# Optimization experiments

Hardware: AMD Instinct MI355X
Metric: run time of the kernel (lower is better)

The kernel has to match this reference:

```python
import jax, jax.numpy as jnp
import numpy as np

NUM_CLUSTERS = 5000  # labels.max()+1, fixed statically for jit
B, K, D, N = 256, 64, 2048, 50000
NHID, H2, NCLASS = 512, 256, 2


def setup_inputs() -> dict:
    key = jax.random.key(0)
    ks = jax.random.split(key, 16)
    s = lambda f_in: 1.0 / np.sqrt(f_in)
    return {
        "indexes": jax.random.randint(ks[0], (B,), 0, N),
        "features": jax.random.normal(ks[1], (N, D), dtype=jnp.float32),
        "labels": jax.random.randint(ks[2], (N,), 0, NUM_CLUSTERS),
        "domain": 1,
        "ori_0": 0,
        "ori_knn_neighbor": jax.random.randint(ks[3], (B, K), 0, N),
        "all_pred": jax.random.normal(ks[4], (B, K, NCLASS), dtype=jnp.float32),
        # GraphConv params (L-GCN style: weight [2*in, out])
        "W1": jax.random.normal(ks[5], (2 * D, NHID), jnp.float32) * s(2 * D),
        "b1": jnp.zeros((NHID,), jnp.float32),
        "W2": jax.random.normal(ks[6], (2 * NHID, H2), jnp.float32) * s(2 * NHID),
        "b2": jnp.zeros((H2,), jnp.float32),
        # classifier: Linear(256,256) -> PReLU(256) -> Linear(256,2)
        "Wc1": jax.random.normal(ks[7], (H2, H2), jnp.float32) * s(H2),
        "bc1": jnp.zeros((H2,), jnp.float32),
        "prelu_a": jnp.full((H2,), 0.25, jnp.float32),
        "Wc2": jax.random.normal(ks[8], (H2, NCLASS), jnp.float32) * s(H2),
        "bc2": jnp.zeros((NCLASS,), jnp.float32),
    }


def _gconv(x, A, W, b):
    # MeanAggregator: bmm(A, x); GraphConv: relu(cat([x, Ax]) @ W + b)
    agg = jnp.einsum('bkj,bjd->bkd', A, x)
    cat = jnp.concatenate([x, agg], axis=-1)
    return jax.nn.relu(jnp.einsum('bkd,df->bkf', cat, W) + b)


def reference(indexes, features, labels, domain, ori_0, ori_knn_neighbor, all_pred,
              W1, b1, W2, b2, Wc1, bc1, prelu_a, Wc2, bc2):
    # ---- cluster mean features (torch: index_add_ then divide; no_grad) ----
    clu_sum = jax.ops.segment_sum(features, labels, num_segments=NUM_CLUSTERS)
    nums = jax.ops.segment_sum(jnp.ones((features.shape[0],), features.dtype),
                               labels, num_segments=NUM_CLUSTERS)
    clu_mean = clu_sum / jnp.maximum(nums, 1.0)[:, None]  # [C, D]

    # ---- batched per-query subgraph construction (vectorized over B) ----
    clu_lab = labels[ori_knn_neighbor]            # [B, K]
    clu_feat = clu_mean[clu_lab]                  # [B, K, D]
    clu_feat = clu_feat.at[:, 0, :].set(features[indexes])  # pivot = raw feature

    A = jnp.einsum('bkd,bjd->bkj', clu_feat, clu_feat)       # pairwise similarity
    A = A * jnp.exp(all_pred[:, :, 1])[:, None, :]           # confidence weighting
    A = jax.nn.softmax(A, axis=-1)                           # row-normalized adjacency

    x = clu_feat / jnp.linalg.norm(clu_feat, axis=-1, keepdims=True)
    x = x - x[:, 0:1, :]                                     # center on pivot

    # (entire construction above is under torch.no_grad)
    x = jax.lax.stop_gradient(x)
    A = jax.lax.stop_gradient(A)

    # ---- GCN layers + classifier ----
    x = _gconv(x, A, W1, b1)      # [B, K, 512]
    x = _gconv(x, A, W2, b2)      # [B, K, 256]
    x0 = x.reshape(-1, H2)        # [B*K, 256]
    h = x0 @ Wc1 + bc1
    h = jnp.where(h >= 0, h, prelu_a * h)  # PReLU(256)
    logits = h @ Wc2 + bc2                 # [B*K, 2]

    # output_feat=True branch
    simm = jnp.sum(clu_mean * clu_mean, axis=1)                   # [C]
    pred = jax.nn.softmax(logits.reshape(B, K, NCLASS), axis=2)   # [B, K, 2]
    return (pred, simm)
```

## Files before the change

kernel.cpp:

```cpp
#include <hip/hip_runtime.h>
#include <math.h>

#define Bq 256
#define Kn 64
#define Dd 2048
#define Nn 50000
#define Cc 5000
#define NHID 512
#define H2d 256
#define LDH 264
#define MP 5376
#define PIVROW 5120
#define LDA1 72

typedef __attribute__((ext_vector_type(8))) __bf16 bf16x8;
typedef __attribute__((ext_vector_type(4))) float f32x4;

__device__ __forceinline__ unsigned short f2bf(float f) {
    union { float f; unsigned int u; } v;
    v.f = f;
    unsigned int u = v.u;
    unsigned int r = (u + 0x7fff + ((u >> 16) & 1)) >> 16;
    return (unsigned short)r;
}
__device__ __forceinline__ float bf2f(unsigned short h) {
    union { unsigned int u; float f; } v;
    v.u = ((unsigned int)h) << 16;
    return v.f;
}

__global__ void k_zero_multi(int* __restrict__ p0, int n0,
                             int* __restrict__ p1, int n1,
                             int* __restrict__ p2, int n2,
                             int* __restrict__ p3, int n3) {
    int i = blockIdx.x * 256 + threadIdx.x;
    if (i < n0) { p0[i] = 0; return; }
    i -= n0;
    if (i < n1) { p1[i] = 0; return; }
    i -= n1;
    if (i < n2) { p2[i] = 0; return; }
    i -= n2;
    if (i < n3) p3[i] = 0;
}

__global__ void k_count(const int* __restrict__ labels, int* __restrict__ cnt, int n) {
    int i = blockIdx.x * 256 + threadIdx.x;
    if (i < n) atomicAdd(&cnt[labels[i]], 1);
}

__global__ void k_alloc(const int* __restrict__ cnt, int* __restrict__ off,
                        int* __restrict__ pos, int* __restrict__ total, int C) {
    int c = blockIdx.x * 256 + threadIdx.x;
    if (c < C) {
        int o = atomicAdd(total, cnt[c]);
        off[c] = o;
        pos[c] = o;
    }
}

__global__ void k_scatter(const int* __restrict__ labels, int* __restrict__ pos,
                          int* __restrict__ rowidx, int n) {
    int i = blockIdx.x * 256 + threadIdx.x;
    if (i < n) {
        int p = atomicAdd(&pos[labels[i]], 1);
        rowidx[p] = i;
    }
}

__global__ __launch_bounds__(256) void k_meansimm(
    const float* __restrict__ feat, const int* __restrict__ rowidx,
    const int* __restrict__ off, const int* __restrict__ cnt,
    const int* __restrict__ indexes,
    float* __restrict__ clu_mean, float* __restrict__ simm,
    unsigned short* __restrict__ PA) {
    int c = blockIdx.x;
    int t = threadIdx.x;
    __shared__ float red[256];

    if (c >= Cc) {
        int b = c - Cc;
        const float* row = feat + (size_t)indexes[b] * Dd;
        float4 v0 = *(const float4*)(row + t * 4);
        float4 v1 = *(const float4*)(row + 1024 + t * 4);
        float ss = v0.x * v0.x + v0.y * v0.y + v0.z * v0.z + v0.w * v0.w +
                   v1.x * v1.x + v1.y * v1.y + v1.z * v1.z + v1.w * v1.w;
        red[t] = ss;
        __syncthreads();
        for (int s2 = 128; s2 > 0; s2 >>= 1) {
            if (t < s2) red[t] += red[t + s2];
            __syncthreads();
        }
        float tot = red[0];
        float rnn = (tot > 0.f) ? rsqrtf(tot) : 0.f;
        ushort4 c0, c1;
        c0.x = f2bf(v0.x * rnn); c0.y = f2bf(v0.y * rnn);
        c0.z = f2bf(v0.z * rnn); c0.w = f2bf(v0.w * rnn);
        c1.x = f2bf(v1.x * rnn); c1.y = f2bf(v1.y * rnn);
        c1.z = f2bf(v1.z * rnn); c1.w = f2bf(v1.w * rnn);
        unsigned short* cr = PA + (size_t)(PIVROW + b) * Dd;
        *(ushort4*)(cr + t * 4) = c0;
        *(ushort4*)(cr + 1024 + t * 4) = c1;
        return;
    }

    int n = cnt[c], st = off[c];
    float4 a0 = {0.f, 0.f, 0.f, 0.f}, a1 = {0.f, 0.f, 0.f, 0.f};
    for (int r = 0; r < n; r++) {
        const float* row = feat + (size_t)rowidx[st + r] * Dd;
        float4 v0 = *(const float4*)(row + t * 4);
        float4 v1 = *(const float4*)(row + 1024 + t * 4);
        a0.x += v0.x; a0.y += v0.y; a0.z += v0.z; a0.w += v0.w;
        a1.x += v1.x; a1.y += v1.y; a1.z += v1.z; a1.w += v1.w;
    }
    float sc = 1.f / (float)(n > 1 ? n : 1);
    a0.x *= sc; a0.y *= sc; a0.z *= sc; a0.w *= sc;
    a1.x *= sc; a1.y *= sc; a1.z *= sc; a1.w *= sc;
    float* outr = clu_mean + (size_t)c * Dd;
    *(float4*)(outr + t * 4) = a0;
    *(float4*)(outr + 1024 + t * 4) = a1;
    float ss = a0.x * a0.x + a0.y * a0.y + a0.z * a0.z + a0.w * a0.w +
               a1.x * a1.x + a1.y * a1.y + a1.z * a1.z + a1.w * a1.w;
    red[t] = ss;
    __syncthreads();
    for (int s2 = 128; s2 > 0; s2 >>= 1) {
        if (t < s2) red[t] += red[t + s2];
        __syncthreads();
    }
    if (t == 0) simm[c] = red[0];
    float tot = red[0];
    float rnn = (tot > 0.f) ? rsqrtf(tot) : 0.f;
    ushort4 c0, c1;
    c0.x = f2bf(a0.x * rnn); c0.y = f2bf(a0.y * rnn);
    c0.z = f2bf(a0.z * rnn); c0.w = f2bf(a0.w * rnn);
    c1.x = f2bf(a1.x * rnn); c1.y = f2bf(a1.y * rnn);
    c1.z = f2bf(a1.z * rnn); c1.w = f2bf(a1.w * rnn);
    unsigned short* cr = PA + (size_t)c * Dd;
    *(ushort4*)(cr + t * 4) = c0;
    *(ushort4*)(cr + 1024 + t * 4) = c1;
}

__global__ __launch_bounds__(512) void k_build_ax(
    const float* __restrict__ feat, const float* __restrict__ clu_mean,
    const int* __restrict__ labels, const int* __restrict__ indexes,
    const int* __restrict__ knn, const float* __restrict__ all_pred,
    float* __restrict__ Abuf) {
    __shared__ unsigned short Hs[64 * LDH];
    __shared__ unsigned short Ls[64 * LDH];
    __shared__ float Gs[64 * 65];
    __shared__ const float* rowp[64];
    __shared__ float wj64[64];

    int b = blockIdx.x, tid = threadIdx.x;
    int wave = tid >> 6, lane = tid & 63, quad = lane >> 4, l16 = lane & 15;
    int rs = (wave >> 1) * 16;
    int cpair = (wave & 1) * 2;

    if (tid < 64) {
        const float* p = (tid == 0) ? feat + (size_t)indexes[b] * Dd
                                    : clu_mean + (size_t)labels[knn[b * 64 + tid]] * Dd;
        rowp[tid] = p;
        wj64[tid] = expf(all_pred[(b * 64 + tid) * 2 + 1]);
    }
    __syncthreads();

    f32x4 acc[2];
#pragma unroll
    for (int j = 0; j < 2; j++) acc[j] = (f32x4){0.f, 0.f, 0.f, 0.f};

    for (int ch = 0; ch < 8; ch++) {
        int d0 = ch * 256;
        __syncthreads();
#pragma unroll
        for (int q = 0; q < 8; q++) {
            int e4 = tid + q * 512;
            int row = e4 >> 6;
            int c4 = (e4 & 63) * 4;
            float4 v = *(const float4*)(rowp[row] + d0 + c4);
            ushort4 h, l;
            h.x = f2bf(v.x); l.x = f2bf(v.x - bf2f(h.x));
            h.y = f2bf(v.y); l.y = f2bf(v.y - bf2f(h.y));
            h.z = f2bf(v.z); l.z = f2bf(v.z - bf2f(h.z));
            h.w = f2bf(v.w); l.w = f2bf(v.w - bf2f(h.w));
            *(ushort4*)&Hs[row * LDH + c4] = h;
            *(ushort4*)&Ls[row * LDH + c4] = l;
        }
        __syncthreads();
#pragma unroll
        for (int ks = 0; ks < 8; ks++) {
            int kk = ks * 32 + quad * 8;
            bf16x8 ah = *(const bf16x8*)&Hs[(rs + l16) * LDH + kk];
            bf16x8 al = *(const bf16x8*)&Ls[(rs + l16) * LDH + kk];
#pragma unroll
            for (int j = 0; j < 2; j++) {
                int jg = cpair + j;
                bf16x8 bh = *(const bf16x8*)&Hs[(jg * 16 + l16) * LDH + kk];
                bf16x8 bl = *(const bf16x8*)&Ls[(jg * 16 + l16) * LDH + kk];
                acc[j] = __builtin_amdgcn_mfma_f32_16x16x32_bf16(ah, bh, acc[j], 0, 0, 0);
                acc[j] = __builtin_amdgcn_mfma_f32_16x16x32_bf16(ah, bl, acc[j], 0, 0, 0);
                acc[j] = __builtin_amdgcn_mfma_f32_16x16x32_bf16(al, bh, acc[j], 0, 0, 0);
            }
        }
    }
    __syncthreads();
#pragma unroll
    for (int j = 0; j < 2; j++)
#pragma unroll
        for (int r = 0; r < 4; r++)
            Gs[(rs + quad * 4 + r) * 65 + (cpair + j) * 16 + l16] = acc[j][r];
    __syncthreads();
    {
        int r = tid >> 3, s = tid & 7;
        float e[8];
        float mx = -1e30f;
#pragma unroll
        for (int c8 = 0; c8 < 8; c8++) {
            int c = s * 8 + c8;
            float v = Gs[r * 65 + c] * wj64[c];
            e[c8] = v;
            mx = fmaxf(mx, v);
        }
        mx = fmaxf(mx, __shfl_xor(mx, 1, 64));
        mx = fmaxf(mx, __shfl_xor(mx, 2, 64));
        mx = fmaxf(mx, __shfl_xor(mx, 4, 64));
        float sum = 0.f;
#pragma unroll
        for (int c8 = 0; c8 < 8; c8++) {
            e[c8] = expf(e[c8] - mx);
            sum += e[c8];
        }
        sum += __shfl_xor(sum, 1, 64);
        sum += __shfl_xor(sum, 2, 64);
        sum += __shfl_xor(sum, 4, 64);
        float inv = 1.f / sum;
        float* Arow = Abuf + ((size_t)b * 64 + r) * 64;
#pragma unroll
        for (int c8 = 0; c8 < 8; c8++) Arow[s * 8 + c8] = e[c8] * inv;
    }
}

__device__ __forceinline__ void pack_item(const float* __restrict__ W,
                                          unsigned short* __restrict__ Bp,
                                          int K, int Nhalf, int split, int idx) {
    int Ntot = split ? 2 * Nhalf : Nhalf;
    int kb = idx / Ntot;
    int n = idx - kb * Ntot;
    float v[8];
#pragma unroll
    for (int j = 0; j < 8; j++) {
        int k = kb * 8 + j;
        if (split)
            v[j] = (n < Nhalf) ? W[(size_t)k * Nhalf + n]
                               : W[(size_t)(K + k) * Nhalf + (n - Nhalf)];
        else
            v[j] = W[(size_t)k * Nhalf + n];
    }
    ushort4 lo, hi;
    lo.x = f2bf(v[0]); lo.y = f2bf(v[1]); lo.z = f2bf(v[2]); lo.w = f2bf(v[3]);
    hi.x = f2bf(v[4]); hi.y = f2bf(v[5]); hi.z = f2bf(v[6]); hi.w = f2bf(v[7]);
    *(ushort4*)&Bp[(size_t)idx * 8] = lo;
    *(ushort4*)&Bp[(size_t)idx * 8 + 4] = hi;
}

__global__ __launch_bounds__(256) void k_pack_all(
    const float* __restrict__ W1, const float* __restrict__ W2,
    const float* __restrict__ Wc1, unsigned short* __restrict__ Bp1,
    unsigned short* __restrict__ Bp2, unsigned short* __restrict__ Bpc) {
    int blk = blockIdx.x;
    int tid = threadIdx.x;
    if (blk < 1024) {
        pack_item(W1, Bp1, Dd, NHID, 1, blk * 256 + tid);
    } else if (blk < 1024 + 128) {
        pack_item(W2, Bp2, 2 * NHID, H2d, 0, (blk - 1024) * 256 + tid);
    } else {
        pack_item(Wc1, Bpc, H2d, H2d, 0, (blk - 1152) * 256 + tid);
    }
}

template <int EPI>
__global__ __launch_bounds__(256) void gemm_bf16_mfma(
    const unsigned short* __restrict__ A, const unsigned short* __restrict__ Bp,
    void* __restrict__ Cout, int M, int K, int N,
    const float* __restrict__ bias, const float* __restrict__ pre_a,
    const float* __restrict__ wc2, float* __restrict__ lbuf) {
    __shared__ unsigned short Asm[128 * 32];
    __shared__ unsigned short Bsm[4 * 128 * 8];
    int tid = threadIdx.x;
    int wave = tid >> 6, lane = tid & 63;
    int quad = lane >> 4, l16 = lane & 15;
    int m0 = blockIdx.y * 128, n0 = blockIdx.x * 128;
    int wm = (wave >> 1) * 64, wn = (wave & 1) * 64;

    f32x4 acc[4][4];
#pragma unroll
    for (int i = 0; i < 4; i++)
#pragma unroll
        for (int j = 0; j < 4; j++) acc[i][j] = (f32x4){0.f, 0.f, 0.f, 0.f};

    int ia0 = wave * 2, ia1 = wave * 2 + 1;
    const unsigned short* gA0 = A + (size_t)(m0 + ia0 * 16 + (lane >> 2)) * K + (lane & 3) * 8;
    const unsigned short* gA1 = gA0 + (size_t)16 * K;
    const unsigned short* gB0 = Bp + (size_t)(n0 + lane) * 8 + (size_t)wave * N * 8;

    for (int k0 = 0; k0 < K; k0 += 32) {
        __syncthreads();
        size_t bko = (size_t)(k0 >> 3) * N * 8;
        __builtin_amdgcn_global_load_lds(
            (const __attribute__((address_space(1))) void*)(gA0 + k0),
            (__attribute__((address_space(3))) void*)(Asm + ia0 * 512), 16, 0, 0);
        __builtin_amdgcn_global_load_lds(
            (const __attribute__((address_space(1))) void*)(gA1 + k0),
            (__attribute__((address_space(3))) void*)(Asm + ia1 * 512), 16, 0, 0);
        __builtin_amdgcn_global_load_lds(
            (const __attribute__((address_space(1))) void*)(gB0 + bko),
            (__attribute__((address_space(3))) void*)(Bsm + wave * 1024), 16, 0, 0);
        __builtin_amdgcn_global_load_lds(
            (const __attribute__((address_space(1))) void*)(gB0 + bko + 512),
            (__attribute__((address_space(3))) void*)(Bsm + wave * 1024 + 512), 16, 0, 0);
        __syncthreads();

        bf16x8 a[4], b[4];
#pragma unroll
        for (int i = 0; i < 4; i++)
            a[i] = *(const bf16x8*)&Asm[(wm + i * 16 + l16) * 32 + quad * 8];
#pragma unroll
        for (int j = 0; j < 4; j++)
            b[j] = *(const bf16x8*)&Bsm[quad * 1024 + (wn + j * 16 + l16) * 8];
#pragma unroll
        for (int i = 0; i < 4; i++)
#pragma unroll
            for (int j = 0; j < 4; j++)
                acc[i][j] = __builtin_amdgcn_mfma_f32_16x16x32_bf16(
                    a[i], b[j], acc[i][j], 0, 0, 0);
    }

    if (EPI == 0) {
        float* C = (float*)Cout;
#pragma unroll
        for (int i = 0; i < 4; i++)
#pragma unroll
            for (int j = 0; j < 4; j++) {
                int col = n0 + wn + j * 16 + l16;
#pragma unroll
                for (int r = 0; r < 4; r++) {
                    int row = m0 + wm + i * 16 + quad * 4 + r;
                    C[(size_t)row * N + col] = acc[i][j][r];
                }
            }
    } else if (EPI == 2) {
        unsigned short* C = (unsigned short*)Cout;
#pragma unroll
        for (int i = 0; i < 4; i++)
#pragma unroll
            for (int j = 0; j < 4; j++) {
                int col = n0 + wn + j * 16 + l16;
                float bcol = bias[col];
#pragma unroll
                for (int r = 0; r < 4; r++) {
                    int row = m0 + wm + i * 16 + quad * 4 + r;
                    float v = acc[i][j][r] + bcol;
                    v = fmaxf(v, 0.f);
                    C[(size_t)row * N + col] = f2bf(v);
                }
            }
    } else {
#pragma unroll
        for (int i = 0; i < 4; i++) {
#pragma unroll
            for (int r = 0; r < 4; r++) {
                float l0 = 0.f, l1 = 0.f;
#pragma unroll
                for (int j = 0; j < 4; j++) {
                    int col = n0 + wn + j * 16 + l16;
                    float v = acc[i][j][r] + bias[col];
                    v = (v >= 0.f) ? v : pre_a[col] * v;
                    l0 += v * wc2[2 * col];
                    l1 += v * wc2[2 * col + 1];
                }
#pragma unroll
                for (int mm = 1; mm < 16; mm <<= 1) {
                    l0 += __shfl_xor(l0, mm, 64);
                    l1 += __shfl_xor(l1, mm, 64);
                }
                if (l16 == 0) {
                    int row = m0 + wm + i * 16 + quad * 4 + r;
                    atomicAdd(&lbuf[2 * row], l0);
                    atomicAdd(&lbuf[2 * row + 1], l1);
                }
            }
        }
    }
}

__global__ __launch_bounds__(256) void k_gcn1(
    const float* __restrict__ P, const float* __restrict__ Abuf,
    const int* __restrict__ labels, const int* __restrict__ knn,
    const float* __restrict__ bias, unsigned short* __restrict__ xy1) {
    __shared__ unsigned short Ah[64 * LDA1], Al[64 * LDA1];
    __shared__ unsigned short Xh[64 * LDA1], Xl[64 * LDA1];
    __shared__ unsigned short Tt[64 * LDA1];
    __shared__ int rowid[64];

    int b = blockIdx.x, hf = blockIdx.y, tid = threadIdx.x;
    int wave = tid >> 6, lane = tid & 63, quad = lane >> 4, l16 = lane & 15;

    if (tid < 64)
        rowid[tid] = (tid == 0) ? (PIVROW + b) : labels[knn[b * 64 + tid]];

    const float* Ab = Abuf + (size_t)b * 64 * 64;
#pragma unroll
    for (int q = 0; q < 4; q++) {
        int e4 = tid + q * 256;
        int row = e4 >> 4;
        int c4 = (e4 & 15) * 4;
        float4 v = *(const float4*)(Ab + row * 64 + c4);
        ushort4 h, l;
        h.x = f2bf(v.x); l.x = f2bf(v.x - bf2f(h.x));
        h.y = f2bf(v.y); l.y = f2bf(v.y - bf2f(h.y));
        h.z = f2bf(v.z); l.z = f2bf(v.z - bf2f(h.z));
        h.w = f2bf(v.w); l.w = f2bf(v.w - bf2f(h.w));
        *(ushort4*)&Ah[row * LDA1 + c4] = h;
        *(ushort4*)&Al[row * LDA1 + c4] = l;
    }

    const float* Q = P + (size_t)(PIVROW + b) * 1024;
    unsigned short* xout = xy1 + (size_t)b * 64 * 1024;

    for (int w = hf * 4; w < hf * 4 + 4; w++) {
        int w0 = w * 64;
        __syncthreads();
#pragma unroll
        for (int q = 0; q < 4; q++) {
            int e4 = tid + q * 256;
            int j = e4 >> 4;
            int c4 = (e4 & 15) * 4;
            float4 v = *(const float4*)(P + (size_t)rowid[j] * 1024 + 512 + w0 + c4);
            float4 qv = *(const float4*)(Q + 512 + w0 + c4);
            v.x -= qv.x; v.y -= qv.y; v.z -= qv.z; v.w -= qv.w;
            unsigned short h;
            h = f2bf(v.x); Xh[(c4 + 0) * LDA1 + j] = h; Xl[(c4 + 0) * LDA1 + j] = f2bf(v.x - bf2f(h));
            h = f2bf(v.y); Xh[(c4 + 1) * LDA1 + j] = h; Xl[(c4 + 1) * LDA1 + j] = f2bf(v.y - bf2f(h));
            h = f2bf(v.z); Xh[(c4 + 2) * LDA1 + j] = h; Xl[(c4 + 2) * LDA1 + j] = f2bf(v.z - bf2f(h));
            h = f2bf(v.w); Xh[(c4 + 3) * LDA1 + j] = h; Xl[(c4 + 3) * LDA1 + j] = f2bf(v.w - bf2f(h));
        }
        __syncthreads();
        f32x4 acc[4];
#pragma unroll
        for (int t = 0; t < 4; t++) acc[t] = (f32x4){0.f, 0.f, 0.f, 0.f};
#pragma unroll
        for (int ks = 0; ks < 2; ks++) {
            int j0 = ks * 32 + quad * 8;
            bf16x8 ah = *(const bf16x8*)&Ah[(wave * 16 + l16) * LDA1 + j0];
            bf16x8 al = *(const bf16x8*)&Al[(wave * 16 + l16) * LDA1 + j0];
#pragma unroll
            for (int t = 0; t < 4; t++) {
                bf16x8 bh = *(const bf16x8*)&Xh[(t * 16 + l16) * LDA1 + j0];
                bf16x8 bl = *(const bf16x8*)&Xl[(t * 16 + l16) * LDA1 + j0];
                acc[t] = __builtin_amdgcn_mfma_f32_16x16x32_bf16(ah, bh, acc[t], 0, 0, 0);
                acc[t] = __builtin_amdgcn_mfma_f32_16x16x32_bf16(ah, bl, acc[t], 0, 0, 0);
                acc[t] = __builtin_amdgcn_mfma_f32_16x16x32_bf16(al, bh, acc[t], 0, 0, 0);
            }
        }
#pragma unroll
        for (int t = 0; t < 4; t++) {
            int cl = t * 16 + l16;
            int c = w0 + cl;
            float bb = bias[c];
            float qa = Q[c];
#pragma unroll
            for (int r = 0; r < 4; r++) {
                int k = wave * 16 + quad * 4 + r;
                float ua = P[(size_t)rowid[k] * 1024 + c] - qa;
                float v = fmaxf(acc[t][r] + ua + bb, 0.f);
                unsigned short hv = f2bf(v);
                xout[(size_t)k * 1024 + c] = hv;
                Tt[cl * LDA1 + k] = hv;
            }
        }
        __syncthreads();
        f32x4 acc2[4];
#pragma unroll
        for (int t = 0; t < 4; t++) acc2[t] = (f32x4){0.f, 0.f, 0.f, 0.f};
#pragma unroll
        for (int ks = 0; ks < 2; ks++) {
            int j0 = ks * 32 + quad * 8;
            bf16x8 ah = *(const bf16x8*)&Ah[(wave * 16 + l16) * LDA1 + j0];
            bf16x8 al = *(const bf16x8*)&Al[(wave * 16 + l16) * LDA1 + j0];
#pragma unroll
            for (int t = 0; t < 4; t++) {
                bf16x8 bh = *(const bf16x8*)&Tt[(t * 16 + l16) * LDA1 + j0];
                acc2[t] = __builtin_amdgcn_mfma_f32_16x16x32_bf16(ah, bh, acc2[t], 0, 0, 0);
                acc2[t] = __builtin_amdgcn_mfma_f32_16x16x32_bf16(al, bh, acc2[t], 0, 0, 0);
            }
        }
#pragma unroll
        for (int t = 0; t < 4; t++) {
            int c = 512 + w0 + t * 16 + l16;
#pragma unroll
            for (int r = 0; r < 4; r++) {
                int k = wave * 16 + quad * 4 + r;
                xout[(size_t)k * 1024 + c] = f2bf(acc2[t][r]);
            }
        }
    }
}

__global__ void k_soft2(const float* __restrict__ lbuf, const float* __restrict__ bc2,
                        float* __restrict__ pred) {
    int m = blockIdx.x * 256 + threadIdx.x;
    if (m < Bq * Kn) {
        float L0 = lbuf[2 * m] + bc2[0];
        float L1 = lbuf[2 * m + 1] + bc2[1];
        float mx = fmaxf(L0, L1);
        float e0 = expf(L0 - mx), e1 = expf(L1 - mx);
        float inv = 1.f / (e0 + e1);
        pred[2 * m] = e0 * inv;
        pred[2 * m + 1] = e1 * inv;
    }
}

extern "C" void kernel_launch(void* const* d_in, const int* in_sizes, int n_in,
                              void* d_out, int out_size, void* d_ws, size_t ws_size,
                              hipStream_t stream) {
    const int* indexes = (const int*)d_in[0];
    const float* features = (const float*)d_in[1];
    const int* labels = (const int*)d_in[2];
    const int* knn = (const int*)d_in[5];
    const float* all_pred = (const float*)d_in[6];
    const float* W1 = (const float*)d_in[7];
    const float* b1 = (const float*)d_in[8];
    const float* W2 = (const float*)d_in[9];
    const float* b2 = (const float*)d_in[10];
    const float* Wc1 = (const float*)d_in[11];
    const float* bc1 = (const float*)d_in[12];
    const float* pre_a = (const float*)d_in[13];
    const float* Wc2 = (const float*)d_in[14];
    const float* bc2 = (const float*)d_in[15];
    float* out = (float*)d_out;

    char* w = (char*)d_ws;
    size_t o = 0;
    auto carve = [&](size_t bytes) -> char* {
        char* p = w + o;
        o += (bytes + 255) & ~(size_t)255;
        return p;
    };
    int* cnt = (int*)carve((size_t)Cc * 4);
    int* off = (int*)carve((size_t)Cc * 4);
    int* pos = (int*)carve((size_t)Cc * 4);
    int* total = (int*)carve(4);
    int* rowidx = (int*)carve((size_t)Nn * 4);
    float* clu_mean = (float*)carve((size_t)Cc * Dd * 4);
    unsigned short* PA = (unsigned short*)carve((size_t)MP * Dd * 2);
    float* Pout = (float*)carve((size_t)MP * 2 * NHID * 4);
    float* Abuf = (float*)carve((size_t)Bq * Kn * Kn * 4);
    unsigned short* Bp1 = (unsigned short*)carve((size_t)(Dd / 8) * 1024 * 8 * 2);
    unsigned short* xy1 = (unsigned short*)carve((size_t)Bq * Kn * 1024 * 2);
    unsigned short* Bp2 = (unsigned short*)carve((size_t)(2 * NHID / 8) * H2d * 8 * 2);
    unsigned short* x2 = (unsigned short*)carve((size_t)Bq * Kn * H2d * 2);
    unsigned short* Bpc = (unsigned short*)carve((size_t)(H2d / 8) * 256 * 8 * 2);
    float* lbuf = (float*)carve((size_t)Bq * Kn * 2 * 4);

    float* simm_out = out + (size_t)Bq * Kn * 2;

    {
        int nPad = (PIVROW - Cc) * Dd / 2;
        int nLb = Bq * Kn * 2;
        int ntot = Cc + nPad + nLb + 1;
        k_zero_multi<<<(ntot + 255) / 256, 256, 0, stream>>>(
            cnt, Cc, (int*)(PA + (size_t)Cc * Dd), nPad, (int*)lbuf, nLb, total, 1);
    }
    k_count<<<(Nn + 255) / 256, 256, 0, stream>>>(labels, cnt, Nn);
    k_alloc<<<(Cc + 255) / 256, 256, 0, stream>>>(cnt, off, pos, total, Cc);
    k_scatter<<<(Nn + 255) / 256, 256, 0, stream>>>(labels, pos, rowidx, Nn);

    k_meansimm<<<Cc + Bq, 256, 0, stream>>>(features, rowidx, off, cnt, indexes,
                                            clu_mean, simm_out, PA);

    k_build_ax<<<Bq, 512, 0, stream>>>(features, clu_mean, labels, indexes, knn,
                                       all_pred, Abuf);

    k_pack_all<<<1184, 256, 0, stream>>>(W1, W2, Wc1, Bp1, Bp2, Bpc);

    {
        dim3 g(1024 / 128, MP / 128);
        gemm_bf16_mfma<0><<<g, 256, 0, stream>>>(PA, Bp1, Pout, MP, Dd, 1024,
                                                 nullptr, nullptr, nullptr, nullptr);
    }
    {
        dim3 g(Bq, 2);
        k_gcn1<<<g, 256, 0, stream>>>(Pout, Abuf, labels, knn, b1, xy1);
    }
    {
        dim3 g(H2d / 128, (Bq * Kn) / 128);
        gemm_bf16_mfma<2><<<g, 256, 0, stream>>>(xy1, Bp2, x2, Bq * Kn, 1024, H2d,
                                                 b2, nullptr, nullptr, nullptr);
    }
    {
        dim3 g(H2d / 128, (Bq * Kn) / 128);
        gemm_bf16_mfma<3><<<g, 256, 0, stream>>>(x2, Bpc, nullptr, Bq * Kn, H2d, H2d,
                                                 bc1, pre_a, Wc2, lbuf);
    }
    k_soft2<<<(Bq * Kn + 255) / 256, 256, 0, stream>>>(lbuf, bc2, out);

    (void)in_sizes; (void)n_in; (void)out_size; (void)ws_size;
}
```

Before: 798.0 us.

## Fuse GCN layer-2 and classifier GEMMs, prepack hi/lo bf16 means, retile kernels

k_meansimm now stores cluster means and pivot features as packed hi/lo bf16 pairs, so k_build_ax only unpacks them and no longer converts from fp32. k_build_ax moves to 1024 threads with one 16x16 tile per wave. The first GEMM uses 64-row tiles to launch more blocks, and k_gcn1 is split over 8 column groups instead of 2. The layer-2 GEMM and the classifier GEMM are fused into one kernel that keeps the intermediate activations in LDS, removing the x2 round trip through global memory. The trade-offs are more per-block LDS and register pressure, plus lower MFMA reuse in the smaller GEMM tiles.

```diff
diff --git a/kernel.cpp b/kernel.cpp
--- a/kernel.cpp
+++ b/kernel.cpp
@@ -12,6 +12,7 @@
 #define MP 5376
 #define PIVROW 5120
 #define LDA1 72
+#define LDX 264
 
 typedef __attribute__((ext_vector_type(8))) __bf16 bf16x8;
 typedef __attribute__((ext_vector_type(4))) float f32x4;
@@ -27,6 +28,11 @@
     union { unsigned int u; float f; } v;
     v.u = ((unsigned int)h) << 16;
     return v.f;
+}
+__device__ __forceinline__ unsigned int hl_pack(float f) {
+    unsigned short h = f2bf(f);
+    unsigned short l = f2bf(f - bf2f(h));
+    return (unsigned int)h | ((unsigned int)l << 16);
 }
 
 __global__ void k_zero_multi(int* __restrict__ p0, int n0,
@@ -71,8 +77,8 @@
     const float* __restrict__ feat, const int* __restrict__ rowidx,
     const int* __restrict__ off, const int* __restrict__ cnt,
     const int* __restrict__ indexes,
-    float* __restrict__ clu_mean, float* __restrict__ simm,
-    unsigned short* __restrict__ PA) {
+    unsigned int* __restrict__ HLm, unsigned int* __restrict__ HLp,
+    float* __restrict__ simm, unsigned short* __restrict__ PA) {
     int c = blockIdx.x;
     int t = threadIdx.x;
     __shared__ float red[256];
@@ -82,6 +88,12 @@
         const float* row = feat + (size_t)indexes[b] * Dd;
         float4 v0 = *(const float4*)(row + t * 4);
         float4 v1 = *(const float4*)(row + 1024 + t * 4);
+        uint4 u0, u1;
+        u0.x = hl_pack(v0.x); u0.y = hl_pack(v0.y); u0.z = hl_pack(v0.z); u0.w = hl_pack(v0.w);
+        u1.x = hl_pack(v1.x); u1.y = hl_pack(v1.y); u1.z = hl_pack(v1.z); u1.w = hl_pack(v1.w);
+        unsigned int* hp = HLp + (size_t)b * Dd;
+        *(uint4*)(hp + t * 4) = u0;
+        *(uint4*)(hp + 1024 + t * 4) = u1;
         float ss = v0.x * v0.x + v0.y * v0.y + v0.z * v0.z + v0.w * v0.w +
                    v1.x * v1.x + v1.y * v1.y + v1.z * v1.z + v1.w * v1.w;
         red[t] = ss;
@@ -115,9 +127,12 @@
     float sc = 1.f / (float)(n > 1 ? n : 1);
     a0.x *= sc; a0.y *= sc; a0.z *= sc; a0.w *= sc;
     a1.x *= sc; a1.y *= sc; a1.z *= sc; a1.w *= sc;
-    float* outr = clu_mean + (size_t)c * Dd;
-    *(float4*)(outr + t * 4) = a0;
-    *(float4*)(outr + 1024 + t * 4) = a1;
+    uint4 u0, u1;
+    u0.x = hl_pack(a0.x); u0.y = hl_pack(a0.y); u0.z = hl_pack(a0.z); u0.w = hl_pack(a0.w);
+    u1.x = hl_pack(a1.x); u1.y = hl_pack(a1.y); u1.z = hl_pack(a1.z); u1.w = hl_pack(a1.w);
+    unsigned int* hm = HLm + (size_t)c * Dd;
+    *(uint4*)(hm + t * 4) = u0;
+    *(uint4*)(hm + 1024 + t * 4) = u1;
     float ss = a0.x * a0.x + a0.y * a0.y + a0.z * a0.z + a0.w * a0.w +
                a1.x * a1.x + a1.y * a1.y + a1.z * a1.z + a1.w * a1.w;
     red[t] = ss;
@@ -139,48 +154,45 @@
     *(ushort4*)(cr + 1024 + t * 4) = c1;
 }
 
-__global__ __launch_bounds__(512) void k_build_ax(
-    const float* __restrict__ feat, const float* __restrict__ clu_mean,
-    const int* __restrict__ labels, const int* __restrict__ indexes,
-    const int* __restrict__ knn, const float* __restrict__ all_pred,
-    float* __restrict__ Abuf) {
+__global__ __launch_bounds__(1024) void k_build_ax(
+    const unsigned int* __restrict__ HLm, const unsigned int* __restrict__ HLp,
+    const int* __restrict__ labels, const int* __restrict__ knn,
+    const float* __restrict__ all_pred, float* __restrict__ Abuf) {
     __shared__ unsigned short Hs[64 * LDH];
     __shared__ unsigned short Ls[64 * LDH];
     __shared__ float Gs[64 * 65];
-    __shared__ const float* rowp[64];
+    __shared__ const unsigned int* rowp[64];
     __shared__ float wj64[64];
 
     int b = blockIdx.x, tid = threadIdx.x;
     int wave = tid >> 6, lane = tid & 63, quad = lane >> 4, l16 = lane & 15;
-    int rs = (wave >> 1) * 16;
-    int cpair = (wave & 1) * 2;
+    int rs = (wave >> 2) * 16;
+    int ct = wave & 3;
 
     if (tid < 64) {
-        const float* p = (tid == 0) ? feat + (size_t)indexes[b] * Dd
-                                    : clu_mean + (size_t)labels[knn[b * 64 + tid]] * Dd;
+        const unsigned int* p = (tid == 0) ? HLp + (size_t)b * Dd
+                                           : HLm + (size_t)labels[knn[b * 64 + tid]] * Dd;
         rowp[tid] = p;
         wj64[tid] = expf(all_pred[(b * 64 + tid) * 2 + 1]);
     }
     __syncthreads();
 
-    f32x4 acc[2];
-#pragma unroll
-    for (int j = 0; j < 2; j++) acc[j] = (f32x4){0.f, 0.f, 0.f, 0.f};
+    f32x4 acc = (f32x4){0.f, 0.f, 0.f, 0.f};
 
     for (int ch = 0; ch < 8; ch++) {
         int d0 = ch * 256;
         __syncthreads();
 #pragma unroll
-        for (int q = 0; q < 8; q++) {
-            int e4 = tid + q * 512;
+        for (int q = 0; q < 4; q++) {
+            int e4 = tid + q * 1024;
             int row = e4 >> 6;
             int c4 = (e4 & 63) * 4;
-            float4 v = *(const float4*)(rowp[row] + d0 + c4);
+            uint4 u = *(const uint4*)(rowp[row] + d0 + c4);
             ushort4 h, l;
-            h.x = f2bf(v.x); l.x = f2bf(v.x - bf2f(h.x));
-            h.y = f2bf(v.y); l.y = f2bf(v.y - bf2f(h.y));
-            h.z = f2bf(v.z); l.z = f2bf(v.z - bf2f(h.z));
-            h.w = f2bf(v.w); l.w = f2bf(v.w - bf2f(h.w));
+            h.x = (unsigned short)(u.x & 0xffff); l.x = (unsigned short)(u.x >> 16);
+            h.y = (unsigned short)(u.y & 0xffff); l.y = (unsigned short)(u.y >> 16);
+            h.z = (unsigned short)(u.z & 0xffff); l.z = (unsigned short)(u.z >> 16);
+            h.w = (unsigned short)(u.w & 0xffff); l.w = (unsigned short)(u.w >> 16);
             *(ushort4*)&Hs[row * LDH + c4] = h;
             *(ushort4*)&Ls[row * LDH + c4] = l;
         }
@@ -190,31 +202,25 @@
             int kk = ks * 32 + quad * 8;
             bf16x8 ah = *(const bf16x8*)&Hs[(rs + l16) * LDH + kk];
             bf16x8 al = *(const bf16x8*)&Ls[(rs + l16) * LDH + kk];
-#pragma unroll
-            for (int j = 0; j < 2; j++) {
-                int jg = cpair + j;
-                bf16x8 bh = *(const bf16x8*)&Hs[(jg * 16 + l16) * LDH + kk];
-                bf16x8 bl = *(const bf16x8*)&Ls[(jg * 16 + l16) * LDH + kk];
-                acc[j] = __builtin_amdgcn_mfma_f32_16x16x32_bf16(ah, bh, acc[j], 0, 0, 0);
-                acc[j] = __builtin_amdgcn_mfma_f32_16x16x32_bf16(ah, bl, acc[j], 0, 0, 0);
-                acc[j] = __builtin_amdgcn_mfma_f32_16x16x32_bf16(al, bh, acc[j], 0, 0, 0);
-            }
+            bf16x8 bh = *(const bf16x8*)&Hs[(ct * 16 + l16) * LDH + kk];
+            bf16x8 bl = *(const bf16x8*)&Ls[(ct * 16 + l16) * LDH + kk];
+            acc = __builtin_amdgcn_mfma_f32_16x16x32_bf16(ah, bh, acc, 0, 0, 0);
+            acc = __builtin_amdgcn_mfma_f32_16x16x32_bf16(ah, bl, acc, 0, 0, 0);
+            acc = __builtin_amdgcn_mfma_f32_16x16x32_bf16(al, bh, acc, 0, 0, 0);
         }
     }
     __syncthreads();
 #pragma unroll
-    for (int j = 0; j < 2; j++)
-#pragma unroll
-        for (int r = 0; r < 4; r++)
-            Gs[(rs + quad * 4 + r) * 65 + (cpair + j) * 16 + l16] = acc[j][r];
+    for (int r = 0; r < 4; r++)
+        Gs[(rs + quad * 4 + r) * 65 + ct * 16 + l16] = acc[r];
     __syncthreads();
     {
-        int r = tid >> 3, s = tid & 7;
-        float e[8];
+        int r = tid >> 4, s = tid & 15;
+        float e[4];
         float mx = -1e30f;
 #pragma unroll
-        for (int c8 = 0; c8 < 8; c8++) {
-            int c = s * 8 + c8;
+        for (int c8 = 0; c8 < 4; c8++) {
+            int c = s * 4 + c8;
             float v = Gs[r * 65 + c] * wj64[c];
             e[c8] = v;
             mx = fmaxf(mx, v);
@@ -222,19 +228,21 @@
         mx = fmaxf(mx, __shfl_xor(mx, 1, 64));
         mx = fmaxf(mx, __shfl_xor(mx, 2, 64));
         mx = fmaxf(mx, __shfl_xor(mx, 4, 64));
+        mx = fmaxf(mx, __shfl_xor(mx, 8, 64));
         float sum = 0.f;
 #pragma unroll
-        for (int c8 = 0; c8 < 8; c8++) {
+        for (int c8 = 0; c8 < 4; c8++) {
             e[c8] = expf(e[c8] - mx);
             sum += e[c8];
         }
         sum += __shfl_xor(sum, 1, 64);
         sum += __shfl_xor(sum, 2, 64);
         sum += __shfl_xor(sum, 4, 64);
+        sum += __shfl_xor(sum, 8, 64);
         float inv = 1.f / sum;
         float* Arow = Abuf + ((size_t)b * 64 + r) * 64;
 #pragma unroll
-        for (int c8 = 0; c8 < 8; c8++) Arow[s * 8 + c8] = e[c8] * inv;
+        for (int c8 = 0; c8 < 4; c8++) Arow[s * 4 + c8] = e[c8] * inv;
     }
 }
 
@@ -276,29 +284,24 @@
     }
 }
 
-template <int EPI>
 __global__ __launch_bounds__(256) void gemm_bf16_mfma(
     const unsigned short* __restrict__ A, const unsigned short* __restrict__ Bp,
-    void* __restrict__ Cout, int M, int K, int N,
-    const float* __restrict__ bias, const float* __restrict__ pre_a,
-    const float* __restrict__ wc2, float* __restrict__ lbuf) {
-    __shared__ unsigned short Asm[128 * 32];
+    float* __restrict__ C, int M, int K, int N) {
+    __shared__ unsigned short Asm[64 * 32];
     __shared__ unsigned short Bsm[4 * 128 * 8];
     int tid = threadIdx.x;
     int wave = tid >> 6, lane = tid & 63;
     int quad = lane >> 4, l16 = lane & 15;
-    int m0 = blockIdx.y * 128, n0 = blockIdx.x * 128;
-    int wm = (wave >> 1) * 64, wn = (wave & 1) * 64;
-
-    f32x4 acc[4][4];
-#pragma unroll
-    for (int i = 0; i < 4; i++)
+    int m0 = blockIdx.y * 64, n0 = blockIdx.x * 128;
+    int wm = (wave >> 1) * 32, wn = (wave & 1) * 64;
+
+    f32x4 acc[2][4];
+#pragma unroll
+    for (int i = 0; i < 2; i++)
 #pragma unroll
         for (int j = 0; j < 4; j++) acc[i][j] = (f32x4){0.f, 0.f, 0.f, 0.f};
 
-    int ia0 = wave * 2, ia1 = wave * 2 + 1;
-    const unsigned short* gA0 = A + (size_t)(m0 + ia0 * 16 + (lane >> 2)) * K + (lane & 3) * 8;
-    const unsigned short* gA1 = gA0 + (size_t)16 * K;
+    const unsigned short* gA0 = A + (size_t)(m0 + wave * 16 + (lane >> 2)) * K + (lane & 3) * 8;
     const unsigned short* gB0 = Bp + (size_t)(n0 + lane) * 8 + (size_t)wave * N * 8;
 
     for (int k0 = 0; k0 < K; k0 += 32) {
@@ -306,10 +309,7 @@
         size_t bko = (size_t)(k0 >> 3) * N * 8;
         __builtin_amdgcn_global_load_lds(
             (const __attribute__((address_space(1))) void*)(gA0 + k0),
-            (__attribute__((address_space(3))) void*)(Asm + ia0 * 512), 16, 0, 0);
-        __builtin_amdgcn_global_load_lds(
-            (const __attribute__((address_space(1))) void*)(gA1 + k0),
-            (__attribute__((address_space(3))) void*)(Asm + ia1 * 512), 16, 0, 0);
+            (__attribute__((address_space(3))) void*)(Asm + wave * 512), 16, 0, 0);
         __builtin_amdgcn_global_load_lds(
             (const __attribute__((address_space(1))) void*)(gB0 + bko),
             (__attribute__((address_space(3))) void*)(Bsm + wave * 1024), 16, 0, 0);
@@ -318,74 +318,152 @@
             (__attribute__((address_space(3))) void*)(Bsm + wave * 1024 + 512), 16, 0, 0);
         __syncthreads();
 
-        bf16x8 a[4], b[4];
-#pragma unroll
-        for (int i = 0; i < 4; i++)
+        bf16x8 a[2], b[4];
+#pragma unroll
+        for (int i = 0; i < 2; i++)
             a[i] = *(const bf16x8*)&Asm[(wm + i * 16 + l16) * 32 + quad * 8];
 #pragma unroll
         for (int j = 0; j < 4; j++)
             b[j] = *(const bf16x8*)&Bsm[quad * 1024 + (wn + j * 16 + l16) * 8];
 #pragma unroll
-        for (int i = 0; i < 4; i++)
+        for (int i = 0; i < 2; i++)
 #pragma unroll
             for (int j = 0; j < 4; j++)
                 acc[i][j] = __builtin_amdgcn_mfma_f32_16x16x32_bf16(
                     a[i], b[j], acc[i][j], 0, 0, 0);
     }
 
-    if (EPI == 0) {
-        float* C = (float*)Cout;
+#pragma unroll
+    for (int i = 0; i < 2; i++)
+#pragma unroll
+        for (int j = 0; j < 4; j++) {
+            int col = n0 + wn + j * 16 + l16;
+#pragma unroll
+            for (int r = 0; r < 4; r++) {
+                int row = m0 + wm + i * 16 + quad * 4 + r;
+                C[(size_t)row * N + col] = acc[i][j][r];
+            }
+        }
+}
+
+__global__ __launch_bounds__(256) void k_gemm23(
+    const unsigned short* __restrict__ A, const unsigned short* __restrict__ Bp2,
+    const unsigned short* __restrict__ Bpc, const float* __restrict__ b2,
+    const float* __restrict__ bc1, const float* __restrict__ pre_a,
+    const float* __restrict__ wc2, float* __restrict__ lbuf) {
+    __shared__ unsigned short Asm[64 * 32];
+    __shared__ unsigned short Bsm[4 * 256 * 8];
+    __shared__ unsigned short Xs[64 * LDX];
+    int tid = threadIdx.x;
+    int wave = tid >> 6, lane = tid & 63;
+    int quad = lane >> 4, l16 = lane & 15;
+    int m0 = blockIdx.x * 64;
+    int wn = wave * 64;
+
+    f32x4 acc[4][4];
+#pragma unroll
+    for (int i = 0; i < 4; i++)
+#pragma unroll
+        for (int j = 0; j < 4; j++) acc[i][j] = (f32x4){0.f, 0.f, 0.f, 0.f};
+
+    const unsigned short* gA0 = A + (size_t)(m0 + wave * 16 + (lane >> 2)) * 1024 + (lane & 3) * 8;
+
+    for (int k0 = 0; k0 < 1024; k0 += 32) {
+        __syncthreads();
+        __builtin_amdgcn_global_load_lds(
+            (const __attribute__((address_space(1))) void*)(gA0 + k0),
+            (__attribute__((address_space(3))) void*)(Asm + wave * 512), 16, 0, 0);
+        const unsigned short* gB = Bp2 + ((size_t)((k0 >> 3) + wave)) * 256 * 8;
+#pragma unroll
+        for (int q = 0; q < 4; q++) {
+            __builtin_amdgcn_global_load_lds(
+                (const __attribute__((address_space(1))) void*)(gB + (q * 64 + lane) * 8),
+                (__attribute__((address_space(3))) void*)(Bsm + wave * 2048 + q * 512),
+                16, 0, 0);
+        }
+        __syncthreads();
+        bf16x8 a[4], b[4];
 #pragma unroll
         for (int i = 0; i < 4; i++)
+            a[i] = *(const bf16x8*)&Asm[(i * 16 + l16) * 32 + quad * 8];
+#pragma unroll
+        for (int j = 0; j < 4; j++)
+            b[j] = *(const bf16x8*)&Bsm[quad * 2048 + (wn + j * 16 + l16) * 8];
+#pragma unroll
+        for (int i = 0; i < 4; i++)
+#pragma unroll
+            for (int j = 0; j < 4; j++)
+                acc[i][j] = __builtin_amdgcn_mfma_f32_16x16x32_bf16(
+                    a[i], b[j], acc[i][j], 0, 0, 0);
+    }
+    __syncthreads();
+#pragma unroll
+    for (int i = 0; i < 4; i++)
+#pragma unroll
+        for (int j = 0; j < 4; j++) {
+            int col = wn + j * 16 + l16;
+            float bcol = b2[col];
+#pragma unroll
+            for (int r = 0; r < 4; r++) {
+                int row = i * 16 + quad * 4 + r;
+                float v = fmaxf(acc[i][j][r] + bcol, 0.f);
+                Xs[row * LDX + col] = f2bf(v);
+            }
+        }
+
+    f32x4 acc2[4][4];
+#pragma unroll
+    for (int i = 0; i < 4; i++)
+#pragma unroll
+        for (int j = 0; j < 4; j++) acc2[i][j] = (f32x4){0.f, 0.f, 0.f, 0.f};
+
+    for (int k0 = 0; k0 < 256; k0 += 32) {
+        __syncthreads();
+        const unsigned short* gB = Bpc + ((size_t)((k0 >> 3) + wave)) * 256 * 8;
+#pragma unroll
+        for (int q = 0; q < 4; q++) {
+            __builtin_amdgcn_global_load_lds(
+                (const __attribute__((address_space(1))) void*)(gB + (q * 64 + lane) * 8),
+                (__attribute__((address_space(3))) void*)(Bsm + wave * 2048 + q * 512),
+                16, 0, 0);
+        }
+        __syncthreads();
+        bf16x8 a[4], b[4];
+#pragma unroll
+        for (int i = 0; i < 4; i++)
+            a[i] = *(const bf16x8*)&Xs[(i * 16 + l16) * LDX + k0 + quad * 8];
+#pragma unroll
+        for (int j = 0; j < 4; j++)
+            b[j] = *(const bf16x8*)&Bsm[quad * 2048 + (wn + j * 16 + l16) * 8];
+#pragma unroll
+        for (int i = 0; i < 4; i++)
+#pragma unroll
+            for (int j = 0; j < 4; j++)
+                acc2[i][j] = __builtin_amdgcn_mfma_f32_16x16x32_bf16(
+                    a[i], b[j], acc2[i][j], 0, 0, 0);
+    }
+#pragma unroll
+    for (int i = 0; i < 4; i++) {
+#pragma unroll
+        for (int r = 0; r < 4; r++) {
+            float l0 = 0.f, l1 = 0.f;
 #pragma unroll
             for (int j = 0; j < 4; j++) {
-                int col = n0 + wn + j * 16 + l16;
-#pragma unroll
-                for (int r = 0; r < 4; r++) {
-                    int row = m0 + wm + i * 16 + quad * 4 + r;
-                    C[(size_t)row * N + col] = acc[i][j][r];
-                }
+                int col = wn + j * 16 + l16;
+                float v = acc2[i][j][r] + bc1[col];
+                v = (v >= 0.f) ? v : pre_a[col] * v;
+                l0 += v * wc2[2 * col];
+                l1 += v * wc2[2 * col + 1];
             }
-    } else if (EPI == 2) {
-        unsigned short* C = (unsigned short*)Cout;
-#pragma unroll
-        for (int i = 0; i < 4; i++)
-#pragma unroll
-            for (int j = 0; j < 4; j++) {
-                int col = n0 + wn + j * 16 + l16;
-                float bcol = bias[col];
-#pragma unroll
-                for (int r = 0; r < 4; r++) {
-                    int row = m0 + wm + i * 16 + quad * 4 + r;
-                    float v = acc[i][j][r] + bcol;
-                    v = fmaxf(v, 0.f);
-                    C[(size_t)row * N + col] = f2bf(v);
-                }
+#pragma unroll
+            for (int mm = 1; mm < 16; mm <<= 1) {
+                l0 += __shfl_xor(l0, mm, 64);
+                l1 += __shfl_xor(l1, mm, 64);
             }
-    } else {
-#pragma unroll
-        for (int i = 0; i < 4; i++) {
-#pragma unroll
-            for (int r = 0; r < 4; r++) {
-                float l0 = 0.f, l1 = 0.f;
-#pragma unroll
-                for (int j = 0; j < 4; j++) {
-                    int col = n0 + wn + j * 16 + l16;
-                    float v = acc[i][j][r] + bias[col];
-                    v = (v >= 0.f) ? v : pre_a[col] * v;
-                    l0 += v * wc2[2 * col];
-                    l1 += v * wc2[2 * col + 1];
-                }
-#pragma unroll
-                for (int mm = 1; mm < 16; mm <<= 1) {
-                    l0 += __shfl_xor(l0, mm, 64);
-                    l1 += __shfl_xor(l1, mm, 64);
-                }
-                if (l16 == 0) {
-                    int row = m0 + wm + i * 16 + quad * 4 + r;
-                    atomicAdd(&lbuf[2 * row], l0);
-                    atomicAdd(&lbuf[2 * row + 1], l1);
-                }
+            if (l16 == 0) {
+                int row = m0 + i * 16 + quad * 4 + r;
+                atomicAdd(&lbuf[2 * row], l0);
+                atomicAdd(&lbuf[2 * row + 1], l1);
             }
         }
     }
@@ -400,8 +478,9 @@
     __shared__ unsigned short Tt[64 * LDA1];
     __shared__ int rowid[64];
 
-    int b = blockIdx.x, hf = blockIdx.y, tid = threadIdx.x;
+    int b = blockIdx.x, w = blockIdx.y, tid = threadIdx.x;
     int wave = tid >> 6, lane = tid & 63, quad = lane >> 4, l16 = lane & 15;
+    int w0 = w * 64;
 
     if (tid < 64)
         rowid[tid] = (tid == 0) ? (PIVROW + b) : labels[knn[b * 64 + tid]];
@@ -425,81 +504,79 @@
     const float* Q = P + (size_t)(PIVROW + b) * 1024;
     unsigned short* xout = xy1 + (size_t)b * 64 * 1024;
 
-    for (int w = hf * 4; w < hf * 4 + 4; w++) {
-        int w0 = w * 64;
-        __syncthreads();
-#pragma unroll
-        for (int q = 0; q < 4; q++) {
-            int e4 = tid + q * 256;
-            int j = e4 >> 4;
-            int c4 = (e4 & 15) * 4;
-            float4 v = *(const float4*)(P + (size_t)rowid[j] * 1024 + 512 + w0 + c4);
-            float4 qv = *(const float4*)(Q + 512 + w0 + c4);
-            v.x -= qv.x; v.y -= qv.y; v.z -= qv.z; v.w -= qv.w;
-            unsigned short h;
-            h = f2bf(v.x); Xh[(c4 + 0) * LDA1 + j] = h; Xl[(c4 + 0) * LDA1 + j] = f2bf(v.x - bf2f(h));
-            h = f2bf(v.y); Xh[(c4 + 1) * LDA1 + j] = h; Xl[(c4 + 1) * LDA1 + j] = f2bf(v.y - bf2f(h));
-            h = f2bf(v.z); Xh[(c4 + 2) * LDA1 + j] = h; Xl[(c4 + 2) * LDA1 + j] = f2bf(v.z - bf2f(h));
-            h = f2bf(v.w); Xh[(c4 + 3) * LDA1 + j] = h; Xl[(c4 + 3) * LDA1 + j] = f2bf(v.w - bf2f(h));
-        }
-        __syncthreads();
-        f32x4 acc[4];
-#pragma unroll
-        for (int t = 0; t < 4; t++) acc[t] = (f32x4){0.f, 0.f, 0.f, 0.f};
-#pragma unroll
-        for (int ks = 0; ks < 2; ks++) {
-            int j0 = ks * 32 + quad * 8;
-            bf16x8 ah = *(const bf16x8*)&Ah[(wave * 16 + l16) * LDA1 + j0];
-            bf16x8 al = *(const bf16x8*)&Al[(wave * 16 + l16) * LDA1 + j0];
-#pragma unroll
-            for (int t = 0; t < 4; t++) {
-                bf16x8 bh = *(const bf16x8*)&Xh[(t * 16 + l16) * LDA1 + j0];
-                bf16x8 bl = *(const bf16x8*)&Xl[(t * 16 + l16) * LDA1 + j0];
-                acc[t] = __builtin_amdgcn_mfma_f32_16x16x32_bf16(ah, bh, acc[t], 0, 0, 0);
-                acc[t] = __builtin_amdgcn_mfma_f32_16x16x32_bf16(ah, bl, acc[t], 0, 0, 0);
-                acc[t] = __builtin_amdgcn_mfma_f32_16x16x32_bf16(al, bh, acc[t], 0, 0, 0);
-            }
-        }
+#pragma unroll
+    for (int q = 0; q < 4; q++) {
+        int e4 = tid + q * 256;
+        int j = e4 >> 4;
+        int c4 = (e4 & 15) * 4;
+        int rid = (j == 0) ? (PIVROW + b) : labels[knn[b * 64 + j]];
+        float4 v = *(const float4*)(P + (size_t)rid * 1024 + 512 + w0 + c4);
+        float4 qv = *(const float4*)(Q + 512 + w0 + c4);
+        v.x -= qv.x; v.y -= qv.y; v.z -= qv.z; v.w -= qv.w;
+        unsigned short h;
+        h = f2bf(v.x); Xh[(c4 + 0) * LDA1 + j] = h; Xl[(c4 + 0) * LDA1 + j] = f2bf(v.x - bf2f(h));
+        h = f2bf(v.y); Xh[(c4 + 1) * LDA1 + j] = h; Xl[(c4 + 1) * LDA1 + j] = f2bf(v.y - bf2f(h));
+        h = f2bf(v.z); Xh[(c4 + 2) * LDA1 + j] = h; Xl[(c4 + 2) * LDA1 + j] = f2bf(v.z - bf2f(h));
+        h = f2bf(v.w); Xh[(c4 + 3) * LDA1 + j] = h; Xl[(c4 + 3) * LDA1 + j] = f2bf(v.w - bf2f(h));
+    }
+    __syncthreads();
+
+    f32x4 acc[4];
+#pragma unroll
+    for (int t = 0; t < 4; t++) acc[t] = (f32x4){0.f, 0.f, 0.f, 0.f};
+#pragma unroll
+    for (int ks = 0; ks < 2; ks++) {
+        int j0 = ks * 32 + quad * 8;
+        bf16x8 ah = *(const bf16x8*)&Ah[(wave * 16 + l16) * LDA1 + j0];
+        bf16x8 al = *(const bf16x8*)&Al[(wave * 16 + l16) * LDA1 + j0];
 #pragma unroll
         for (int t = 0; t < 4; t++) {
-            int cl = t * 16 + l16;
-            int c = w0 + cl;
-            float bb = bias[c];
-            float qa = Q[c];
-#pragma unroll
-            for (int r = 0; r < 4; r++) {
-                int k = wave * 16 + quad * 4 + r;
-                float ua = P[(size_t)rowid[k] * 1024 + c] - qa;
-                float v = fmaxf(acc[t][r] + ua + bb, 0.f);
-                unsigned short hv = f2bf(v);
-                xout[(size_t)k * 1024 + c] = hv;
-                Tt[cl * LDA1 + k] = hv;
-            }
-        }
-        __syncthreads();
-        f32x4 acc2[4];
-#pragma unroll
-        for (int t = 0; t < 4; t++) acc2[t] = (f32x4){0.f, 0.f, 0.f, 0.f};
-#pragma unroll
-        for (int ks = 0; ks < 2; ks++) {
-            int j0 = ks * 32 + quad * 8;
-            bf16x8 ah = *(const bf16x8*)&Ah[(wave * 16 + l16) * LDA1 + j0];
-            bf16x8 al = *(const bf16x8*)&Al[(wave * 16 + l16) * LDA1 + j0];
-#pragma unroll
-            for (int t = 0; t < 4; t++) {
-                bf16x8 bh = *(const bf16x8*)&Tt[(t * 16 + l16) * LDA1 + j0];
-                acc2[t] = __builtin_amdgcn_mfma_f32_16x16x32_bf16(ah, bh, acc2[t], 0, 0, 0);
-                acc2[t] = __builtin_amdgcn_mfma_f32_16x16x32_bf16(al, bh, acc2[t], 0, 0, 0);
-            }
-        }
+            bf16x8 bh = *(const bf16x8*)&Xh[(t * 16 + l16) * LDA1 + j0];
+            bf16x8 bl = *(const bf16x8*)&Xl[(t * 16 + l16) * LDA1 + j0];
+            acc[t] = __builtin_amdgcn_mfma_f32_16x16x32_bf16(ah, bh, acc[t], 0, 0, 0);
+            acc[t] = __builtin_amdgcn_mfma_f32_16x16x32_bf16(ah, bl, acc[t], 0, 0, 0);
+            acc[t] = __builtin_amdgcn_mfma_f32_16x16x32_bf16(al, bh, acc[t], 0, 0, 0);
+        }
+    }
+#pragma unroll
+    for (int t = 0; t < 4; t++) {
+        int cl = t * 16 + l16;
+        int c = w0 + cl;
+        float bb = bias[c];
+        float qa = Q[c];
+#pragma unroll
+        for (int r = 0; r < 4; r++) {
+            int k = wave * 16 + quad * 4 + r;
+            float ua = P[(size_t)rowid[k] * 1024 + c] - qa;
+            float v = fmaxf(acc[t][r] + ua + bb, 0.f);
+            unsigned short hv = f2bf(v);
+            xout[(size_t)k * 1024 + c] = hv;
+            Tt[cl * LDA1 + k] = hv;
+        }
+    }
+    __syncthreads();
+    f32x4 acc2[4];
+#pragma unroll
+    for (int t = 0; t < 4; t++) acc2[t] = (f32x4){0.f, 0.f, 0.f, 0.f};
+#pragma unroll
+    for (int ks = 0; ks < 2; ks++) {
+        int j0 = ks * 32 + quad * 8;
+        bf16x8 ah = *(const bf16x8*)&Ah[(wave * 16 + l16) * LDA1 + j0];
+        bf16x8 al = *(const bf16x8*)&Al[(wave * 16 + l16) * LDA1 + j0];
 #pragma unroll
         for (int t = 0; t < 4; t++) {
-            int c = 512 + w0 + t * 16 + l16;
-#pragma unroll
-            for (int r = 0; r < 4; r++) {
-                int k = wave * 16 + quad * 4 + r;
-                xout[(size_t)k * 1024 + c] = f2bf(acc2[t][r]);
-            }
+            bf16x8 bh = *(const bf16x8*)&Tt[(t * 16 + l16) * LDA1 + j0];
+            acc2[t] = __builtin_amdgcn_mfma_f32_16x16x32_bf16(ah, bh, acc2[t], 0, 0, 0);
+            acc2[t] = __builtin_amdgcn_mfma_f32_16x16x32_bf16(al, bh, acc2[t], 0, 0, 0);
+        }
+    }
+#pragma unroll
+    for (int t = 0; t < 4; t++) {
+        int c = 512 + w0 + t * 16 + l16;
+#pragma unroll
+        for (int r = 0; r < 4; r++) {
+            int k = wave * 16 + quad * 4 + r;
+            xout[(size_t)k * 1024 + c] = f2bf(acc2[t][r]);
         }
     }
 }
@@ -549,14 +626,14 @@
     int* pos = (int*)carve((size_t)Cc * 4);
     int* total = (int*)carve(4);
     int* rowidx = (int*)carve((size_t)Nn * 4);
-    float* clu_mean = (float*)carve((size_t)Cc * Dd * 4);
+    unsigned int* HLm = (unsigned int*)carve((size_t)Cc * Dd * 4);
+    unsigned int* HLp = (unsigned int*)carve((size_t)Bq * Dd * 4);
     unsigned short* PA = (unsigned short*)carve((size_t)MP * Dd * 2);
     float* Pout = (float*)carve((size_t)MP * 2 * NHID * 4);
     float* Abuf = (float*)carve((size_t)Bq * Kn * Kn * 4);
     unsigned short* Bp1 = (unsigned short*)carve((size_t)(Dd / 8) * 1024 * 8 * 2);
     unsigned short* xy1 = (unsigned short*)carve((size_t)Bq * Kn * 1024 * 2);
     unsigned short* Bp2 = (unsigned short*)carve((size_t)(2 * NHID / 8) * H2d * 8 * 2);
-    unsigned short* x2 = (unsigned short*)carve((size_t)Bq * Kn * H2d * 2);
     unsigned short* Bpc = (unsigned short*)carve((size_t)(H2d / 8) * 256 * 8 * 2);
     float* lbuf = (float*)carve((size_t)Bq * Kn * 2 * 4);
 
@@ -574,32 +651,22 @@
     k_scatter<<<(Nn + 255) / 256, 256, 0, stream>>>(labels, pos, rowidx, Nn);
 
     k_meansimm<<<Cc + Bq, 256, 0, stream>>>(features, rowidx, off, cnt, indexes,
-                                            clu_mean, simm_out, PA);
-
-    k_build_ax<<<Bq, 512, 0, stream>>>(features, clu_mean, labels, indexes, knn,
-                                       all_pred, Abuf);
+                                            HLm, HLp, simm_out, PA);
+
+    k_build_ax<<<Bq, 1024, 0, stream>>>(HLm, HLp, labels, knn, all_pred, Abuf);
 
     k_pack_all<<<1184, 256, 0, stream>>>(W1, W2, Wc1, Bp1, Bp2, Bpc);
 
     {
-        dim3 g(1024 / 128, MP / 128);
-        gemm_bf16_mfma<0><<<g, 256, 0, stream>>>(PA, Bp1, Pout, MP, Dd, 1024,
-                                                 nullptr, nullptr, nullptr, nullptr);
+        dim3 g(1024 / 128, MP / 64);
+        gemm_bf16_mfma<<<g, 256, 0, stream>>>(PA, Bp1, Pout, MP, Dd, 1024);
     }
     {
-        dim3 g(Bq, 2);
+        dim3 g(Bq, 8);
         k_gcn1<<<g, 256, 0, stream>>>(Pout, Abuf, labels, knn, b1, xy1);
     }
-    {
-        dim3 g(H2d / 128, (Bq * Kn) / 128);
-        gemm_bf16_mfma<2><<<g, 256, 0, stream>>>(xy1, Bp2, x2, Bq * Kn, 1024, H2d,
-                                                 b2, nullptr, nullptr, nullptr);
-    }
-    {
-        dim3 g(H2d / 128, (Bq * Kn) / 128);
-        gemm_bf16_mfma<3><<<g, 256, 0, stream>>>(x2, Bpc, nullptr, Bq * Kn, H2d, H2d,
-                                                 bc1, pre_a, Wc2, lbuf);
-    }
+    k_gemm23<<<Bq * Kn / 64, 256, 0, stream>>>(xy1, Bp2, Bpc, b2, bc1, pre_a, Wc2, lbuf);
+
     k_soft2<<<(Bq * Kn + 255) / 256, 256, 0, stream>>>(lbuf, bc2, out);
 
     (void)in_sizes; (void)n_in; (void)out_size; (void)ws_size;
```

After: 756.4 us. 5.2% less time.
